# Kernel tuning notes

Measured on AMD Instinct MI355X. Metric: run time of the kernel, lower is better.

## Reference

```python
import jax, jax.numpy as jnp
import numpy as np

N_NODES = 100000
N_EDGES = 1250000
D = 64


def setup_inputs() -> dict:
    key = jax.random.key(0)
    ks = jax.random.split(key, 5)
    x = jax.random.normal(ks[0], (N_NODES, D), dtype=jnp.float32)
    edge_index = jax.random.randint(ks[1], (2, N_EDGES), 0, N_NODES, dtype=jnp.int64)
    # Linear weights stored as [in, out] so y = x @ W + b
    scale = 1.0 / np.sqrt(D)
    W1 = jax.random.normal(ks[2], (D, D), dtype=jnp.float32) * scale
    b1 = jnp.zeros((D,), dtype=jnp.float32)
    W2 = jax.random.normal(ks[3], (D, D), dtype=jnp.float32) * scale
    b2 = jnp.zeros((D,), dtype=jnp.float32)
    return {"x": x, "edge_index": edge_index, "W1": W1, "b1": b1, "W2": W2, "b2": b2}


def reference(x, edge_index, W1, b1, W2, b2):
    # GINConv with default eps=0: h_i = MLP((1+eps)*x_i + sum_{j in N(i)} x_j)
    src, dst = edge_index[0], edge_index[1]
    # gather source features, scatter-add into destination nodes
    agg = jax.ops.segment_sum(x[src], dst, num_segments=x.shape[0])  # [N, D]
    h = x + agg  # (1 + eps) * x + agg, eps = 0
    # 2-layer MLP: Linear -> ReLU -> Linear
    h = jax.nn.relu(h @ W1 + b1)
    return h @ W2 + b2
```

## Files before the change

### kernel.cpp

```cpp
#include <hip/hip_runtime.h>

#define D 64
#define SCAN_CHUNK 1024
#define NXCD 8
#define NPB 192
#define NBMAX 1024
#define CAP 4096
#define ECHUNK 4096
#define EPB (ECHUNK / 256)
#define HSTR 72
#define DEGMAX 64
#define DEGSTR 65

typedef unsigned short ushort_t;
typedef __bf16 bf16_t;
typedef __bf16 bf16x8 __attribute__((ext_vector_type(8)));
typedef float f32x4 __attribute__((ext_vector_type(4)));
typedef ushort_t ushort8 __attribute__((ext_vector_type(8)));

__device__ __forceinline__ ushort_t f2bf(float v) {
    unsigned u = __float_as_uint(v);
    return (ushort_t)((u + 0x7FFF + ((u >> 16) & 1)) >> 16);
}
__device__ __forceinline__ float bf2f(ushort_t h) {
    return __uint_as_float((unsigned)h << 16);
}


__global__ __launch_bounds__(256) void sort_cast_kernel(const int* __restrict__ src,
                                                        const int* __restrict__ dst,
                                                        int* __restrict__ gcnt,
                                                        unsigned* __restrict__ buf,
                                                        const float4* __restrict__ x4,
                                                        ushort4* __restrict__ xh4,
                                                        int n4,
                                                        const float* __restrict__ W1,
                                                        const float* __restrict__ W2,
                                                        ushort_t* __restrict__ w1t,
                                                        ushort_t* __restrict__ w2t,
                                                        int nEdges, int nB, int cap,
                                                        int nSortB, int nCastB) {
    __shared__ uint2 sp[ECHUNK];
    __shared__ int lhist[NBMAX];
    __shared__ int lofs[NBMAX];
    __shared__ int lbase[NBMAX];
    __shared__ int lcur[NBMAX];
    __shared__ int wsum[4];

    int tid = threadIdx.x;

    if (blockIdx.x >= nSortB) {
        int cb = blockIdx.x - nSortB;
        if (cb == nCastB) {
#pragma unroll
            for (int i = 0; i < 16; i++) {
                int idx = i * 256 + tid;
                int k = idx >> 6, n = idx & 63;
                w1t[n * 64 + k] = f2bf(W1[idx]);
                w2t[n * 64 + k] = f2bf(W2[idx]);
            }
            return;
        }
        int gid = cb * 512 + tid;
        if (gid < n4) {
            float4 v = x4[gid];
            ushort4 o;
            o.x = f2bf(v.x); o.y = f2bf(v.y); o.z = f2bf(v.z); o.w = f2bf(v.w);
            xh4[gid] = o;
        }
        int gid2 = gid + 256;
        if (gid2 < n4) {
            float4 v = x4[gid2];
            ushort4 o;
            o.x = f2bf(v.x); o.y = f2bf(v.y); o.z = f2bf(v.z); o.w = f2bf(v.w);
            xh4[gid2] = o;
        }
        return;
    }

    int lane = tid & 63;
    int wave = tid >> 6;
    int e0 = blockIdx.x * ECHUNK;
    int cnt = min(ECHUNK, nEdges - e0);

    for (int i = tid; i < nB; i += 256) lhist[i] = 0;
    __syncthreads();

    int es[EPB], ed[EPB];
#pragma unroll
    for (int j = 0; j < EPB; j++) {
        int ii = tid + j * 256;
        if (ii < cnt) {
            es[j] = src[e0 + ii];
            ed[j] = dst[e0 + ii];
            atomicAdd(&lhist[ed[j] / NPB], 1);
        } else {
            ed[j] = -1;
        }
    }
    __syncthreads();

    int G = (nB + 255) / 256;
    int b0 = tid * G;
    int tsum = 0;
    for (int j = 0; j < G; j++) {
        int b = b0 + j;
        if (b < nB) tsum += lhist[b];
    }
    int incl = tsum;
#pragma unroll
    for (int dd = 1; dd < 64; dd <<= 1) {
        int t2 = __shfl_up(incl, dd, 64);
        if (lane >= dd) incl += t2;
    }
    if (lane == 63) wsum[wave] = incl;
    __syncthreads();
    int wo = 0;
#pragma unroll
    for (int w = 0; w < 4; w++)
        if (w < wave) wo += wsum[w];
    int run = wo + incl - tsum;
    for (int j = 0; j < G; j++) {
        int b = b0 + j;
        if (b < nB) {
            int h = lhist[b];
            lofs[b] = run;
            lcur[b] = run;
            if (h > 0) lbase[b] = atomicAdd(&gcnt[b], h);
            run += h;
        }
    }
    __syncthreads();

#pragma unroll
    for (int j = 0; j < EPB; j++) {
        if (ed[j] >= 0) {
            int b = ed[j] / NPB;
            int p = atomicAdd(&lcur[b], 1);
            sp[p] = make_uint2((unsigned)es[j], (unsigned)ed[j]);
        }
    }
    __syncthreads();

    for (int i = tid; i < cnt; i += 256) {
        uint2 pr = sp[i];
        int b = (int)pr.y / NPB;
        int idx = lbase[b] + (i - lofs[b]);
        unsigned pk = pr.x | ((pr.y - (unsigned)b * NPB) << 24);
        if (idx < cap) buf[(size_t)b * cap + idx] = pk;
    }
}

__global__ __launch_bounds__(256) void csr_agg_mlp_kernel(const ushort_t* __restrict__ xh,
                                                          const unsigned* __restrict__ buf,
                                                          const int* __restrict__ gcnt,
                                                          const ushort_t* __restrict__ w1t,
                                                          const ushort_t* __restrict__ w2t,
                                                          const float* __restrict__ b1,
                                                          const float* __restrict__ b2,
                                                          float* __restrict__ out,
                                                          int nNodes) {
    __shared__ int ssort[64 * DEGSTR];
    __shared__ int deg[64];
    __shared__ ushort_t ht[4][16 * HSTR];

    int tid = threadIdx.x;
    int base = blockIdx.x * 64;
    int bkt = base / NPB;
    int blo = bkt * NPB;
    int roff = blo - base;

    if (tid < 64) deg[tid] = 0;
    __syncthreads();
    {
        int cnt = min(gcnt[bkt], CAP);
        const unsigned* bp = buf + (size_t)bkt * CAP;
        int cnt4 = cnt & ~3;
        for (int i = tid * 4; i < cnt4; i += 1024) {
            uint4 v4 = *(const uint4*)(bp + i);
#pragma unroll
            for (int k = 0; k < 4; k++) {
                unsigned v = (&v4.x)[k];
                int r = (int)(v >> 24) + roff;
                if ((unsigned)r < 64u) {
                    int p = atomicAdd(&deg[r], 1);
                    if (p < DEGMAX) ssort[r * DEGSTR + p] = (int)(v & 0xFFFFFFu);
                }
            }
        }
        if (tid < (cnt - cnt4)) {
            unsigned v = bp[cnt4 + tid];
            int r = (int)(v >> 24) + roff;
            if ((unsigned)r < 64u) {
                int p = atomicAdd(&deg[r], 1);
                if (p < DEGMAX) ssort[r * DEGSTR + p] = (int)(v & 0xFFFFFFu);
            }
        }
    }
    __syncthreads();

    {
        int nl = tid >> 2;
        int q = tid & 3;
        int n = min(base + nl, nNodes - 1);
        int f = q * 16;
        const ushort_t* xr = xh + (size_t)n * D + f;

        float acc[16];
        ushort8 sv0 = *(const ushort8*)(xr);
        ushort8 sv1 = *(const ushort8*)(xr + 8);
#pragma unroll
        for (int j = 0; j < 8; j++) {
            acc[j] = bf2f(sv0[j]);
            acc[8 + j] = bf2f(sv1[j]);
        }

        int dg = min(deg[nl], DEGMAX);
        const int* el = ssort + nl * DEGSTR;
        int e = 0;
        for (; e + 4 <= dg; e += 4) {
            int s0 = el[e];
            int s1 = el[e + 1];
            int s2 = el[e + 2];
            int s3 = el[e + 3];
            const ushort_t* p0 = xh + (size_t)s0 * D + f;
            const ushort_t* p1 = xh + (size_t)s1 * D + f;
            const ushort_t* p2 = xh + (size_t)s2 * D + f;
            const ushort_t* p3 = xh + (size_t)s3 * D + f;
            ushort8 a0 = *(const ushort8*)(p0);
            ushort8 a0b = *(const ushort8*)(p0 + 8);
            ushort8 a1 = *(const ushort8*)(p1);
            ushort8 a1b = *(const ushort8*)(p1 + 8);
            ushort8 a2 = *(const ushort8*)(p2);
            ushort8 a2b = *(const ushort8*)(p2 + 8);
            ushort8 a3 = *(const ushort8*)(p3);
            ushort8 a3b = *(const ushort8*)(p3 + 8);
#pragma unroll
            for (int j = 0; j < 8; j++) {
                acc[j]     += (bf2f(a0[j]) + bf2f(a1[j])) + (bf2f(a2[j]) + bf2f(a3[j]));
                acc[8 + j] += (bf2f(a0b[j]) + bf2f(a1b[j])) + (bf2f(a2b[j]) + bf2f(a3b[j]));
            }
        }
        for (; e + 2 <= dg; e += 2) {
            int s0 = el[e];
            int s1 = el[e + 1];
            const ushort_t* p0 = xh + (size_t)s0 * D + f;
            const ushort_t* p1 = xh + (size_t)s1 * D + f;
            ushort8 a0 = *(const ushort8*)(p0);
            ushort8 b0 = *(const ushort8*)(p0 + 8);
            ushort8 a1 = *(const ushort8*)(p1);
            ushort8 b1v = *(const ushort8*)(p1 + 8);
#pragma unroll
            for (int j = 0; j < 8; j++) {
                acc[j] += bf2f(a0[j]) + bf2f(a1[j]);
                acc[8 + j] += bf2f(b0[j]) + bf2f(b1v[j]);
            }
        }
        if (e < dg) {
            int s = el[e];
            const ushort_t* p = xh + (size_t)s * D + f;
            ushort8 a = *(const ushort8*)(p);
            ushort8 bb = *(const ushort8*)(p + 8);
#pragma unroll
            for (int j = 0; j < 8; j++) {
                acc[j] += bf2f(a[j]);
                acc[8 + j] += bf2f(bb[j]);
            }
        }

        ushort8 o0, o1;
#pragma unroll
        for (int j = 0; j < 8; j++) {
            o0[j] = f2bf(acc[j]);
            o1[j] = f2bf(acc[8 + j]);
        }
        ushort_t* hr = ht[tid >> 6] + (nl & 15) * HSTR + f;
        *(ushort8*)(hr) = o0;
        *(ushort8*)(hr + 8) = o1;
    }

    int lane = tid & 63;
    int wave = tid >> 6;
    int quad = lane >> 4;
    int col = lane & 15;

    bf16x8 w1f[4][2], w2f[4][2];
#pragma unroll
    for (int nt = 0; nt < 4; nt++)
#pragma unroll
        for (int ks = 0; ks < 2; ks++) {
            int nn = nt * 16 + col;
            w1f[nt][ks] = *(const bf16x8*)(w1t + nn * 64 + ks * 32 + quad * 8);
            w2f[nt][ks] = *(const bf16x8*)(w2t + nn * 64 + ks * 32 + quad * 8);
        }
    float bb1[4], bb2[4];
#pragma unroll
    for (int nt = 0; nt < 4; nt++) {
        bb1[nt] = b1[nt * 16 + col];
        bb2[nt] = b2[nt * 16 + col];
    }

    ushort_t* tw = ht[wave];
    bf16x8 a0 = *(const bf16x8*)(tw + col * HSTR + quad * 8);
    bf16x8 a1 = *(const bf16x8*)(tw + col * HSTR + 32 + quad * 8);

    f32x4 c;
#pragma unroll
    for (int nt = 0; nt < 4; nt++) {
        c = (f32x4){0.f, 0.f, 0.f, 0.f};
        c = __builtin_amdgcn_mfma_f32_16x16x32_bf16(a0, w1f[nt][0], c, 0, 0, 0);
        c = __builtin_amdgcn_mfma_f32_16x16x32_bf16(a1, w1f[nt][1], c, 0, 0, 0);
#pragma unroll
        for (int r = 0; r < 4; r++) {
            float v = fmaxf(c[r] + bb1[nt], 0.0f);
            int m = quad * 4 + r;
            tw[m * HSTR + nt * 16 + col] = f2bf(v);
        }
    }
    bf16x8 d0 = *(const bf16x8*)(tw + col * HSTR + quad * 8);
    bf16x8 d1 = *(const bf16x8*)(tw + col * HSTR + 32 + quad * 8);
#pragma unroll
    for (int nt = 0; nt < 4; nt++) {
        c = (f32x4){0.f, 0.f, 0.f, 0.f};
        c = __builtin_amdgcn_mfma_f32_16x16x32_bf16(d0, w2f[nt][0], c, 0, 0, 0);
        c = __builtin_amdgcn_mfma_f32_16x16x32_bf16(d1, w2f[nt][1], c, 0, 0, 0);
#pragma unroll
        for (int r = 0; r < 4; r++) {
            int row = base + wave * 16 + quad * 4 + r;
            if (row < nNodes) out[(size_t)row * D + nt * 16 + col] = c[r] + bb2[nt];
        }
    }
}

__global__ __launch_bounds__(256) void zero_kernel(int* __restrict__ p, int n) {
    int gid = blockIdx.x * 256 + threadIdx.x;
    if (gid < n) p[gid] = 0;
}

__global__ __launch_bounds__(256) void hist_xcd_kernel(const int* __restrict__ dst,
                                                       int* __restrict__ counts,
                                                       int nEdges, int nNodes,
                                                       int blocksPerXcd) {
    int xcd = blockIdx.x % NXCD;
    int slice = blockIdx.x / NXCD;
    int lo = (int)((long long)nNodes * xcd / NXCD);
    int hi = (int)((long long)nNodes * (xcd + 1) / NXCD);
    int per = (nEdges + blocksPerXcd - 1) / blocksPerXcd;
    int e0 = slice * per;
    int e1 = min(e0 + per, nEdges);
    for (int e = e0 + (int)threadIdx.x; e < e1; e += 256) {
        int d = dst[e];
        if (d >= lo && d < hi) atomicAdd(&counts[d], 1);
    }
}

__global__ __launch_bounds__(256) void scan_reduce_kernel(const int* __restrict__ counts,
                                                          int* __restrict__ blockSums,
                                                          int nNodes) {
    __shared__ int ws[4];
    int base = blockIdx.x * SCAN_CHUNK;
    int tid = threadIdx.x;
    int s = 0;
#pragma unroll
    for (int i = 0; i < 4; i++) {
        int idx = base + tid + 256 * i;
        if (idx < nNodes) s += counts[idx];
    }
#pragma unroll
    for (int d = 32; d > 0; d >>= 1) s += __shfl_xor(s, d, 64);
    if ((tid & 63) == 0) ws[tid >> 6] = s;
    __syncthreads();
    if (tid == 0) blockSums[blockIdx.x] = ws[0] + ws[1] + ws[2] + ws[3];
}

__global__ __launch_bounds__(256) void scan_sums_kernel(int* __restrict__ blockSums,
                                                        int* __restrict__ off,
                                                        int nSB, int nNodes, int nEdges) {
    __shared__ int ws[4];
    int tid = threadIdx.x;
    int lane = tid & 63;
    int wave = tid >> 6;
    int v = (tid < nSB) ? blockSums[tid] : 0;
    int incl = v;
#pragma unroll
    for (int d = 1; d < 64; d <<= 1) {
        int t = __shfl_up(incl, d, 64);
        if (lane >= d) incl += t;
    }
    if (lane == 63) ws[wave] = incl;
    __syncthreads();
    int waveOff = 0;
#pragma unroll
    for (int w = 0; w < 4; w++)
        if (w < wave) waveOff += ws[w];
    if (tid < nSB) blockSums[tid] = waveOff + incl - v;
    if (tid == 0) off[nNodes] = nEdges;
}

__global__ __launch_bounds__(1024) void scan_write_kernel(int* __restrict__ off,
                                                          int* __restrict__ cur,
                                                          const int* __restrict__ blockSums,
                                                          int nNodes) {
    __shared__ int waveSums[16];
    int tid = threadIdx.x;
    int lane = tid & 63;
    int wave = tid >> 6;
    int i = blockIdx.x * SCAN_CHUNK + tid;
    int v = (i < nNodes) ? off[i] : 0;
    int incl = v;
#pragma unroll
    for (int d = 1; d < 64; d <<= 1) {
        int t = __shfl_up(incl, d, 64);
        if (lane >= d) incl += t;
    }
    if (lane == 63) waveSums[wave] = incl;
    __syncthreads();
    if (wave == 0) {
        int wv = (lane < 16) ? waveSums[lane] : 0;
        int s = wv;
#pragma unroll
        for (int d = 1; d < 16; d <<= 1) {
            int t = __shfl_up(s, d, 64);
            if (lane >= d) s += t;
        }
        if (lane < 16) waveSums[lane] = s - wv;
    }
    __syncthreads();
    if (i < nNodes) {
        int excl = blockSums[blockIdx.x] + waveSums[wave] + incl - v;
        off[i] = excl;
        cur[i] = excl;
    }
}

__global__ __launch_bounds__(256) void fill_xcd_kernel(const int* __restrict__ src,
                                                       const int* __restrict__ dst,
                                                       int* __restrict__ cur,
                                                       int* __restrict__ ssrc,
                                                       int nEdges, int nNodes,
                                                       int blocksPerXcd) {
    int xcd = blockIdx.x % NXCD;
    int slice = blockIdx.x / NXCD;
    int lo = (int)((long long)nNodes * xcd / NXCD);
    int hi = (int)((long long)nNodes * (xcd + 1) / NXCD);
    int per = (nEdges + blocksPerXcd - 1) / blocksPerXcd;
    int e0 = slice * per;
    int e1 = min(e0 + per, nEdges);
    for (int e = e0 + (int)threadIdx.x; e < e1; e += 256) {
        int d = dst[e];
        if (d >= lo && d < hi) {
            int p = atomicAdd(&cur[d], 1);
            ssrc[p] = src[e];
        }
    }
}

__global__ __launch_bounds__(256) void aggregate_kernel(const float* __restrict__ x,
                                                        const int* __restrict__ off,
                                                        const int* __restrict__ ssrc,
                                                        float* __restrict__ out,
                                                        int nNodes) {
    int gid = blockIdx.x * 256 + threadIdx.x;
    int n = gid >> 4;
    if (n >= nNodes) return;
    int f = (gid & 15) * 4;
    float4 acc = *(const float4*)(x + (size_t)n * D + f);
    int e0 = off[n], e1 = off[n + 1];
    for (int e = e0; e < e1; e++) {
        int s = ssrc[e];
        float4 v = *(const float4*)(x + (size_t)s * D + f);
        acc.x += v.x; acc.y += v.y; acc.z += v.z; acc.w += v.w;
    }
    *(float4*)(out + (size_t)n * D + f) = acc;
}

__global__ __launch_bounds__(256) void mlp_reg_kernel(const float* hin,
                                                      const float* __restrict__ W1,
                                                      const float* __restrict__ b1,
                                                      const float* __restrict__ W2,
                                                      const float* __restrict__ b2,
                                                      float* out,
                                                      int nNodes) {
    int lane = threadIdx.x & 63;
    int wave = threadIdx.x >> 6;
    float w1[D], w2[D];
#pragma unroll
    for (int k = 0; k < D; k++) w1[k] = W1[k * D + lane];
#pragma unroll
    for (int k = 0; k < D; k++) w2[k] = W2[k * D + lane];
    float bb1 = b1[lane];
    float bb2 = b2[lane];
    int gw = blockIdx.x * 4 + wave;
    int nW = gridDim.x * 4;
    for (int n = gw; n < nNodes; n += nW) {
        float hv = hin[(size_t)n * D + lane];
        float a0 = bb1, a1 = 0.0f, a2 = 0.0f, a3 = 0.0f;
#pragma unroll
        for (int k = 0; k < D; k += 4) {
            float h0 = __uint_as_float(__builtin_amdgcn_readlane(__float_as_uint(hv), k + 0));
            float h1 = __uint_as_float(__builtin_amdgcn_readlane(__float_as_uint(hv), k + 1));
            float h2 = __uint_as_float(__builtin_amdgcn_readlane(__float_as_uint(hv), k + 2));
            float h3 = __uint_as_float(__builtin_amdgcn_readlane(__float_as_uint(hv), k + 3));
            a0 = fmaf(h0, w1[k + 0], a0);
            a1 = fmaf(h1, w1[k + 1], a1);
            a2 = fmaf(h2, w1[k + 2], a2);
            a3 = fmaf(h3, w1[k + 3], a3);
        }
        float m = fmaxf((a0 + a1) + (a2 + a3), 0.0f);
        float c0 = bb2, c1 = 0.0f, c2 = 0.0f, c3 = 0.0f;
#pragma unroll
        for (int k = 0; k < D; k += 4) {
            float h0 = __uint_as_float(__builtin_amdgcn_readlane(__float_as_uint(m), k + 0));
            float h1 = __uint_as_float(__builtin_amdgcn_readlane(__float_as_uint(m), k + 1));
            float h2 = __uint_as_float(__builtin_amdgcn_readlane(__float_as_uint(m), k + 2));
            float h3 = __uint_as_float(__builtin_amdgcn_readlane(__float_as_uint(m), k + 3));
            c0 = fmaf(h0, w2[k + 0], c0);
            c1 = fmaf(h1, w2[k + 1], c1);
            c2 = fmaf(h2, w2[k + 2], c2);
            c3 = fmaf(h3, w2[k + 3], c3);
        }
        out[(size_t)n * D + lane] = (c0 + c1) + (c2 + c3);
    }
}

extern "C" void kernel_launch(void* const* d_in, const int* in_sizes, int n_in,
                              void* d_out, int out_size, void* d_ws, size_t ws_size,
                              hipStream_t stream) {
    const float* x  = (const float*)d_in[0];
    const int*   ei = (const int*)d_in[1];
    const float* W1 = (const float*)d_in[2];
    const float* b1 = (const float*)d_in[3];
    const float* W2 = (const float*)d_in[4];
    const float* b2 = (const float*)d_in[5];
    float* out = (float*)d_out;

    const int nNodes = in_sizes[0] / D;
    const int nEdges = in_sizes[1] / 2;
    const int* src = ei;
    const int* dst = ei + nEdges;

    const int NB = (nNodes + NPB - 1) / NPB;

    int* gcnt = (int*)d_ws;
    unsigned* buf = (unsigned*)(gcnt + 1024);
    ushort_t* xh  = (ushort_t*)(buf + (size_t)NB * CAP);
    ushort_t* w1t = xh + (size_t)nNodes * D;
    ushort_t* w2t = w1t + 4096;

    size_t wsT0 = (size_t)1024 * 4
                + (size_t)NB * CAP * 4
                + (size_t)nNodes * D * 2 + 2 * 4096 * 2;
    bool tier0 = (ws_size >= wsT0) && (NB <= NBMAX) && (nNodes > 0)
              && (nNodes < (1 << 24))
              && ((long long)nEdges * NPB / nNodes * 14 / 10 < CAP)
              && ((long long)nEdges * 2 / nNodes < DEGMAX);

    if (tier0) {
        int n4 = nNodes * (D / 4);
        int nSortB = (nEdges + ECHUNK - 1) / ECHUNK;
        int nCastB = (n4 + 511) / 512;
        hipMemsetAsync(gcnt, 0, 1024 * sizeof(int), stream);
        sort_cast_kernel<<<nSortB + nCastB + 1, 256, 0, stream>>>(
            src, dst, gcnt, buf, (const float4*)x, (ushort4*)xh, n4,
            W1, W2, w1t, w2t, nEdges, NB, CAP, nSortB, nCastB);
        int nG = (nNodes + 63) / 64;
        csr_agg_mlp_kernel<<<nG, 256, 0, stream>>>(
            xh, buf, gcnt, w1t, w2t, b1, b2, out, nNodes);
        return;
    }

    const int nSB = (nNodes + SCAN_CHUNK - 1) / SCAN_CHUNK;
    int* foff  = (int*)d_ws;
    int* fcur  = foff + (nNodes + 1);
    int* fssrc = fcur + nNodes;
    int* fsums = fssrc + nEdges;

    zero_kernel<<<(nNodes + 1 + 255) / 256, 256, 0, stream>>>(foff, nNodes + 1);
    {
        const int blocksPerXcd = 256;
        hist_xcd_kernel<<<blocksPerXcd * NXCD, 256, 0, stream>>>(
            dst, foff, nEdges, nNodes, blocksPerXcd);
    }
    scan_reduce_kernel<<<nSB, 256, 0, stream>>>(foff, fsums, nNodes);
    scan_sums_kernel<<<1, 256, 0, stream>>>(fsums, foff, nSB, nNodes, nEdges);
    scan_write_kernel<<<nSB, 1024, 0, stream>>>(foff, fcur, fsums, nNodes);
    {
        const int blocksPerXcd = 256;
        fill_xcd_kernel<<<blocksPerXcd * NXCD, 256, 0, stream>>>(
            src, dst, fcur, fssrc, nEdges, nNodes, blocksPerXcd);
    }
    long long work = (long long)nNodes * 16;
    aggregate_kernel<<<(int)((work + 255) / 256), 256, 0, stream>>>(x, foff, fssrc, out, nNodes);
    mlp_reg_kernel<<<6250, 256, 0, stream>>>(out, W1, b1, W2, b2, out, nNodes);
}
```

Baseline: 149.3 us.

## Use 512-thread sort blocks and XCD-aware block remapping in aggregation kernel

Raises the sort/cast kernel block size from 256 to 512 threads, halving per-thread edge registers and the cast block count. It also remaps block IDs in the aggregation+MLP kernel so consecutive node groups land on the same XCD, aiming for better L2 locality of the shared bucket buffers. The remap changes which blocks share a bucket's buffer, and larger blocks may reduce occupancy given the heavy LDS use.

```diff
diff --git a/kernel.cpp b/kernel.cpp
--- a/kernel.cpp
+++ b/kernel.cpp
@@ -7,7 +7,8 @@
 #define NBMAX 1024
 #define CAP 4096
 #define ECHUNK 4096
-#define EPB (ECHUNK / 256)
+#define SBT 512
+#define EPB (ECHUNK / SBT)
 #define HSTR 72
 #define DEGMAX 64
 #define DEGSTR 65
@@ -27,7 +28,7 @@
 }
 
 
-__global__ __launch_bounds__(256) void sort_cast_kernel(const int* __restrict__ src,
+__global__ __launch_bounds__(SBT) void sort_cast_kernel(const int* __restrict__ src,
                                                         const int* __restrict__ dst,
                                                         int* __restrict__ gcnt,
                                                         unsigned* __restrict__ buf,
@@ -45,7 +46,7 @@
     __shared__ int lofs[NBMAX];
     __shared__ int lbase[NBMAX];
     __shared__ int lcur[NBMAX];
-    __shared__ int wsum[4];
+    __shared__ int wsum[SBT / 64];
 
     int tid = threadIdx.x;
 
@@ -53,22 +54,22 @@
         int cb = blockIdx.x - nSortB;
         if (cb == nCastB) {
 #pragma unroll
-            for (int i = 0; i < 16; i++) {
-                int idx = i * 256 + tid;
+            for (int i = 0; i < 8; i++) {
+                int idx = i * SBT + tid;
                 int k = idx >> 6, n = idx & 63;
                 w1t[n * 64 + k] = f2bf(W1[idx]);
                 w2t[n * 64 + k] = f2bf(W2[idx]);
             }
             return;
         }
-        int gid = cb * 512 + tid;
+        int gid = cb * (2 * SBT) + tid;
         if (gid < n4) {
             float4 v = x4[gid];
             ushort4 o;
             o.x = f2bf(v.x); o.y = f2bf(v.y); o.z = f2bf(v.z); o.w = f2bf(v.w);
             xh4[gid] = o;
         }
-        int gid2 = gid + 256;
+        int gid2 = gid + SBT;
         if (gid2 < n4) {
             float4 v = x4[gid2];
             ushort4 o;
@@ -83,13 +84,13 @@
     int e0 = blockIdx.x * ECHUNK;
     int cnt = min(ECHUNK, nEdges - e0);
 
-    for (int i = tid; i < nB; i += 256) lhist[i] = 0;
+    for (int i = tid; i < nB; i += SBT) lhist[i] = 0;
     __syncthreads();
 
     int es[EPB], ed[EPB];
 #pragma unroll
     for (int j = 0; j < EPB; j++) {
-        int ii = tid + j * 256;
+        int ii = tid + j * SBT;
         if (ii < cnt) {
             es[j] = src[e0 + ii];
             ed[j] = dst[e0 + ii];
@@ -100,7 +101,7 @@
     }
     __syncthreads();
 
-    int G = (nB + 255) / 256;
+    int G = (nB + SBT - 1) / SBT;
     int b0 = tid * G;
     int tsum = 0;
     for (int j = 0; j < G; j++) {
@@ -117,7 +118,7 @@
     __syncthreads();
     int wo = 0;
 #pragma unroll
-    for (int w = 0; w < 4; w++)
+    for (int w = 0; w < SBT / 64; w++)
         if (w < wave) wo += wsum[w];
     int run = wo + incl - tsum;
     for (int j = 0; j < G; j++) {
@@ -142,7 +143,7 @@
     }
     __syncthreads();
 
-    for (int i = tid; i < cnt; i += 256) {
+    for (int i = tid; i < cnt; i += SBT) {
         uint2 pr = sp[i];
         int b = (int)pr.y / NPB;
         int idx = lbase[b] + (i - lofs[b]);
@@ -165,7 +166,13 @@
     __shared__ ushort_t ht[4][16 * HSTR];
 
     int tid = threadIdx.x;
-    int base = blockIdx.x * 64;
+    int nwg = gridDim.x;
+    int orig = blockIdx.x;
+    int xcd = orig & (NXCD - 1);
+    int idx8 = orig >> 3;
+    int q = nwg >> 3, r = nwg & (NXCD - 1);
+    int wgid = (xcd < r ? xcd * (q + 1) : r * (q + 1) + (xcd - r) * q) + idx8;
+    int base = wgid * 64;
     int bkt = base / NPB;
     int blo = bkt * NPB;
     int roff = blo - base;
@@ -181,19 +188,19 @@
 #pragma unroll
             for (int k = 0; k < 4; k++) {
                 unsigned v = (&v4.x)[k];
-                int r = (int)(v >> 24) + roff;
-                if ((unsigned)r < 64u) {
-                    int p = atomicAdd(&deg[r], 1);
-                    if (p < DEGMAX) ssort[r * DEGSTR + p] = (int)(v & 0xFFFFFFu);
+                int r2 = (int)(v >> 24) + roff;
+                if ((unsigned)r2 < 64u) {
+                    int p = atomicAdd(&deg[r2], 1);
+                    if (p < DEGMAX) ssort[r2 * DEGSTR + p] = (int)(v & 0xFFFFFFu);
                 }
             }
         }
         if (tid < (cnt - cnt4)) {
             unsigned v = bp[cnt4 + tid];
-            int r = (int)(v >> 24) + roff;
-            if ((unsigned)r < 64u) {
-                int p = atomicAdd(&deg[r], 1);
-                if (p < DEGMAX) ssort[r * DEGSTR + p] = (int)(v & 0xFFFFFFu);
+            int r2 = (int)(v >> 24) + roff;
+            if ((unsigned)r2 < 64u) {
+                int p = atomicAdd(&deg[r2], 1);
+                if (p < DEGMAX) ssort[r2 * DEGSTR + p] = (int)(v & 0xFFFFFFu);
             }
         }
     }
@@ -201,9 +208,9 @@
 
     {
         int nl = tid >> 2;
-        int q = tid & 3;
+        int q2 = tid & 3;
         int n = min(base + nl, nNodes - 1);
-        int f = q * 16;
+        int f = q2 * 16;
         const ushort_t* xr = xh + (size_t)n * D + f;
 
         float acc[16];
@@ -311,9 +318,9 @@
         c = __builtin_amdgcn_mfma_f32_16x16x32_bf16(a0, w1f[nt][0], c, 0, 0, 0);
         c = __builtin_amdgcn_mfma_f32_16x16x32_bf16(a1, w1f[nt][1], c, 0, 0, 0);
 #pragma unroll
-        for (int r = 0; r < 4; r++) {
-            float v = fmaxf(c[r] + bb1[nt], 0.0f);
-            int m = quad * 4 + r;
+        for (int r2 = 0; r2 < 4; r2++) {
+            float v = fmaxf(c[r2] + bb1[nt], 0.0f);
+            int m = quad * 4 + r2;
             tw[m * HSTR + nt * 16 + col] = f2bf(v);
         }
     }
@@ -325,9 +332,9 @@
         c = __builtin_amdgcn_mfma_f32_16x16x32_bf16(d0, w2f[nt][0], c, 0, 0, 0);
         c = __builtin_amdgcn_mfma_f32_16x16x32_bf16(d1, w2f[nt][1], c, 0, 0, 0);
 #pragma unroll
-        for (int r = 0; r < 4; r++) {
-            int row = base + wave * 16 + quad * 4 + r;
-            if (row < nNodes) out[(size_t)row * D + nt * 16 + col] = c[r] + bb2[nt];
+        for (int r2 = 0; r2 < 4; r2++) {
+            int row = base + wave * 16 + quad * 4 + r2;
+            if (row < nNodes) out[(size_t)row * D + nt * 16 + col] = c[r2] + bb2[nt];
         }
     }
 }
@@ -558,9 +565,9 @@
     if (tier0) {
         int n4 = nNodes * (D / 4);
         int nSortB = (nEdges + ECHUNK - 1) / ECHUNK;
-        int nCastB = (n4 + 511) / 512;
+        int nCastB = (n4 + 2 * SBT - 1) / (2 * SBT);
         hipMemsetAsync(gcnt, 0, 1024 * sizeof(int), stream);
-        sort_cast_kernel<<<nSortB + nCastB + 1, 256, 0, stream>>>(
+        sort_cast_kernel<<<nSortB + nCastB + 1, SBT, 0, stream>>>(
             src, dst, gcnt, buf, (const float4*)x, (ushort4*)xh, n4,
             W1, W2, w1t, w2t, nEdges, NB, CAP, nSortB, nCastB);
         int nG = (nNodes + 63) / 64;
```

After: 141.9 us. 5.0% less time.
